# Performance work log

Hardware: AMD Instinct MI355X
Metric: run time of the kernel (lower is better)

## Reference

```python
import jax, jax.numpy as jnp
import numpy as np

B, L, C, K = 4, 32768, 64, 7
NORM_FACTOR = 1.0
EPS = 1e-5


def setup_inputs() -> dict:
    key = jax.random.key(0)
    ks = jax.random.split(key, 7)
    return {
        "x": jax.random.normal(ks[0], (B, L, C), jnp.float32),
        "weights": jax.random.normal(ks[1], (C, C, K), jnp.float32) * 0.05,  # ~lecun scale
        "w_conv": jax.random.normal(ks[2], (C, C), jnp.float32) * 0.125,
        "scale1": jax.random.uniform(ks[3], (C,), jnp.float32, 0.5, 1.5),
        "bias1": jax.random.normal(ks[4], (C,), jnp.float32) * 0.1,
        "scale2": jax.random.uniform(ks[5], (C,), jnp.float32, 0.5, 1.5),
        "bias2": jax.random.normal(ks[6], (C,), jnp.float32) * 0.1,
    }


def _batchnorm(x, scale, bias):
    # train-mode BatchNorm: stats over (batch, length), feature axis last
    mean = jnp.mean(x, axis=(0, 1), keepdims=True)
    var = jnp.var(x, axis=(0, 1), keepdims=True)
    return (x - mean) * jax.lax.rsqrt(var + EPS) * scale + bias


def reference(x, weights, w_conv, scale1, bias1, scale2, bias2):
    b, l, c = x.shape
    k = weights.shape[-1]
    x_ = x
    # unfold: windows of 2K at stride 2 -> (B, C*2K, T) -> (B, C, T, 2K)
    p = jax.lax.conv_general_dilated_patches(
        jnp.transpose(x, (0, 2, 1)), filter_shape=(2 * k,),
        window_strides=(2,), padding=((0, 0),))
    t = p.shape[-1]
    xp = jnp.transpose(jnp.reshape(p, (b, c, 2 * k, t)), (0, 1, 3, 2))
    # dynamic gate weights: (B, 2T, C) x (Cout, Cin, K) -> (B, Cout, 2T, K)
    w = jnp.einsum('blc,dck->bdlk', x_[:, -(2 * t):, :], weights)
    even_seq = w[:, :, ::2, :]   # (B, C, T, K)
    odd_seq = w[:, :, 1::2, :]   # (B, C, T, K)
    w = jnp.reshape(jnp.stack([even_seq, odd_seq], axis=-1), (b, c, t, 2 * k))
    w = jnp.tanh(w / NORM_FACTOR)
    y = jnp.sum(xp * w, axis=3)            # (B, C, T)
    y = jnp.transpose(y, (0, 2, 1))        # (B, T, C)
    y = x_[:, ::2, :][:, -t:, :] + y       # skip and inner_skip
    y = _batchnorm(y, scale1, bias1)
    y_ = y
    z = y @ w_conv                          # 1x1 conv, no bias
    z = _batchnorm(z, scale2, bias2)
    z = jax.nn.gelu(z)                      # approximate=True, matches flax default
    return y_ + z
```

## Files before the change

kernel.cpp:

```cpp
#include <hip/hip_runtime.h>
#include <hip/hip_bf16.h>

#define B_ 4
#define L_ 32768
#define C_ 64
#define K_ 7
#define T_ 16378
#define M_ (B_*T_)
#define TJ 16
#define IT 4
#define NJB 256
#define NBLKA (B_*NJB)
#define NBZ 512
#define NBE 1024

#define OF_WB   0
#define OF_WB2  14336
#define OF_Y    16384
#define OF_PS1  (OF_Y + M_*32)
#define OF_PQ1  (OF_PS1 + 64*NBLKA)
#define OF_PS2  (OF_PQ1 + 64*NBLKA)
#define OF_PQ2  (OF_PS2 + 64*NBZ)
#define OF_C1   (OF_PQ2 + 64*NBZ)
#define OF_C2   (OF_C1 + 128)

typedef __attribute__((ext_vector_type(8))) short short8;
typedef __attribute__((ext_vector_type(4))) float f32x4;

__device__ __forceinline__ unsigned cvt_pk_bf16(float a, float b) {
    unsigned r;
    asm("v_cvt_pk_bf16_f32 %0, %1, %2" : "=v"(r) : "v"(a), "v"(b));
    return r;
}

__device__ __forceinline__ float fast_tanh(float x) {
    float e = __builtin_amdgcn_exp2f(x * 2.885390082f);
    return __builtin_fmaf(-2.f, __builtin_amdgcn_rcpf(1.f + e), 1.f);
}

__device__ __forceinline__ float gelu_tanh(float v) {
    float u = 0.7978845608028654f * (v + 0.044715f * v * v * v);
    return 0.5f * v * (1.f + fast_tanh(u));
}

__device__ __forceinline__ float bfu(ushort h) {
    union { unsigned u; float f; } v; v.u = ((unsigned)h) << 16; return v.f;
}
__device__ __forceinline__ float bflo(unsigned p) {
    union { unsigned u; float f; } v; v.u = p << 16; return v.f;
}

__global__ void kPb(const float* __restrict__ w, ushort* __restrict__ Wb) {
    int i = blockIdx.x * 256 + threadIdx.x;
    if (i < 28672) {
        int j = i & 7;
        int l = (i >> 3) & 63;
        int q = i >> 9;
        int nt = q % 28, kt = q / 28;
        int k = kt * 32 + 8 * (l >> 4) + j;
        int n = nt * 16 + (l & 15);
        int d = n / 7, kk = n - 7 * d;
        Wb[i] = (ushort)(cvt_pk_bf16(w[(d * 64 + k) * 7 + kk], 0.f) & 0xffffu);
    }
}

__global__ __launch_bounds__(256, 4) void kA(const float* __restrict__ x,
                                             const ushort* __restrict__ Wb,
                                             ushort* __restrict__ y,
                                             float* __restrict__ ps,
                                             float* __restrict__ pq) {
    __shared__ ushort xp[22 * 128];
    __shared__ ushort gsT[448 * 36];
    __shared__ float  red[2][4][64];

    const int tid = threadIdx.x;
    const int w = tid >> 6, l = tid & 63;
    const int b = blockIdx.y;
    const float* xb = x + (long)b * L_ * 64;

    short8 wreg[7][2];
    #pragma unroll
    for (int i = 0; i < 7; ++i) {
        wreg[i][0] = *(const short8*)&Wb[((w + 4 * i) * 64 + l) * 8];
        wreg[i][1] = *(const short8*)&Wb[((28 + w + 4 * i) * 64 + l) * 8];
    }

    float S = 0.f, Q = 0.f;

    for (int it = 0; it < IT; ++it) {
        const int jt = blockIdx.x * IT + it;
        const int j0 = jt * TJ;
        const int xrow0 = 2 * j0;
        if (it) __syncthreads();

        #pragma unroll
        for (int st = 0; st < 3; ++st) {
            int p = tid + st * 256;
            if (p < 704) {
                int rp = p >> 5, c0 = (p & 31) * 2;
                int r0 = min(xrow0 + 2 * rp, L_ - 1);
                int r1 = min(xrow0 + 2 * rp + 1, L_ - 1);
                float2 va = *(const float2*)(xb + (long)r0 * 64 + c0);
                float2 vb = *(const float2*)(xb + (long)r1 * 64 + c0);
                uint2 wv;
                wv.x = cvt_pk_bf16(va.x, vb.x);
                wv.y = cvt_pk_bf16(va.y, vb.y);
                *(uint2*)((char*)xp + rp * 256 + c0 * 4) = wv;
            }
        }

        short8 afr[2][2];
        #pragma unroll
        for (int mt = 0; mt < 2; ++mt)
            #pragma unroll
            for (int kt = 0; kt < 2; ++kt) {
                int row = min(xrow0 + 12 + mt * 16 + (l & 15), L_ - 1);
                const float* pr = xb + (long)row * 64 + kt * 32 + (l >> 4) * 8;
                float4 v0 = *(const float4*)pr;
                float4 v1 = *(const float4*)(pr + 4);
                uint4 u;
                u.x = cvt_pk_bf16(v0.x, v0.y);
                u.y = cvt_pk_bf16(v0.z, v0.w);
                u.z = cvt_pk_bf16(v1.x, v1.y);
                u.w = cvt_pk_bf16(v1.z, v1.w);
                afr[mt][kt] = *(short8*)&u;
            }

        {
            const int col = l & 15;
            const int r0 = 4 * (l >> 4);
            #pragma unroll
            for (int i = 0; i < 7; ++i) {
                const int nt = w + 4 * i;
                f32x4 acc0 = {0.f, 0.f, 0.f, 0.f};
                f32x4 acc1 = {0.f, 0.f, 0.f, 0.f};
                acc0 = __builtin_amdgcn_mfma_f32_16x16x32_bf16(afr[0][0], wreg[i][0], acc0, 0, 0, 0);
                acc0 = __builtin_amdgcn_mfma_f32_16x16x32_bf16(afr[0][1], wreg[i][1], acc0, 0, 0, 0);
                acc1 = __builtin_amdgcn_mfma_f32_16x16x32_bf16(afr[1][0], wreg[i][0], acc1, 0, 0, 0);
                acc1 = __builtin_amdgcn_mfma_f32_16x16x32_bf16(afr[1][1], wreg[i][1], acc1, 0, 0, 0);
                const int n = nt * 16 + col;
                char* base = (char*)gsT + n * 72;
                uint2 lo, hi;
                lo.x = cvt_pk_bf16(fast_tanh(acc0[0]), fast_tanh(acc0[1]));
                lo.y = cvt_pk_bf16(fast_tanh(acc0[2]), fast_tanh(acc0[3]));
                hi.x = cvt_pk_bf16(fast_tanh(acc1[0]), fast_tanh(acc1[1]));
                hi.y = cvt_pk_bf16(fast_tanh(acc1[2]), fast_tanh(acc1[3]));
                *(uint2*)(base + r0 * 2)      = lo;
                *(uint2*)(base + 32 + r0 * 2) = hi;
            }
        }
        __syncthreads();

        #pragma unroll
        for (int jp = 0; jp < 2; ++jp) {
            const int jj0 = 2 * w + 8 * jp;
            unsigned xv[8];
            #pragma unroll
            for (int k2 = 0; k2 < 8; ++k2)
                xv[k2] = *(const unsigned*)((const char*)xp + (jj0 + k2) * 256 + l * 4);
            float acc0 = bflo(xv[6]);
            float acc1 = bflo(xv[7]);
            const char* gbp = (const char*)gsT + l * 504 + jj0 * 4;
            #pragma unroll
            for (int kk = 0; kk < K_; ++kk) {
                uint2 gp = *(const uint2*)(gbp + kk * 72);
                asm("v_dot2_f32_bf16 %0, %1, %2, %0" : "+v"(acc0) : "v"(xv[kk]),     "v"(gp.x));
                asm("v_dot2_f32_bf16 %0, %1, %2, %0" : "+v"(acc1) : "v"(xv[kk + 1]), "v"(gp.y));
            }
            float o0 = __shfl_xor(acc0, 1);
            float o1 = __shfl_xor(acc1, 1);
            const int j = j0 + jj0;
            if (j < T_) {
                if ((l & 1) == 0) {
                    *(unsigned*)((char*)y + (long)(b * T_ + j) * 128 + l * 2)     = cvt_pk_bf16(acc0, o0);
                    *(unsigned*)((char*)y + (long)(b * T_ + j + 1) * 128 + l * 2) = cvt_pk_bf16(acc1, o1);
                }
                S += acc0 + acc1;
                Q += acc0 * acc0 + acc1 * acc1;
            }
        }
    }

    red[0][w][l] = S;
    red[1][w][l] = Q;
    __syncthreads();
    if (tid < 64) {
        float S4 = red[0][0][tid] + red[0][1][tid] + red[0][2][tid] + red[0][3][tid];
        float Q4 = red[1][0][tid] + red[1][1][tid] + red[1][2][tid] + red[1][3][tid];
        int blk = b * NJB + blockIdx.x;
        ps[tid * NBLKA + blk] = S4;
        pq[tid * NBLKA + blk] = Q4;
    }
}

__global__ void kB(const float* __restrict__ ps, const float* __restrict__ pq,
                   float* __restrict__ A, float* __restrict__ BB,
                   const float* __restrict__ scale, const float* __restrict__ bias,
                   int nblk, float invN) {
    const int c = blockIdx.x;
    const float* bs = ps + (long)c * nblk;
    const float* bq = pq + (long)c * nblk;
    float S = 0.f, Q = 0.f;
    for (int i = threadIdx.x; i < nblk; i += 256) {
        S += bs[i];
        Q += bq[i];
    }
    for (int o = 32; o > 0; o >>= 1) {
        S += __shfl_down(S, o);
        Q += __shfl_down(Q, o);
    }
    __shared__ float rs[4], rq[4];
    if ((threadIdx.x & 63) == 0) { rs[threadIdx.x >> 6] = S; rq[threadIdx.x >> 6] = Q; }
    __syncthreads();
    if (threadIdx.x == 0) {
        S = rs[0] + rs[1] + rs[2] + rs[3];
        Q = rq[0] + rq[1] + rq[2] + rq[3];
        float m = S * invN;
        float var = Q * invN - m * m;
        float rstd = rsqrtf(var + 1e-5f);
        float a = rstd * scale[c];
        A[c] = a;
        BB[c] = bias[c] - m * a;
    }
}

__global__ void kW(const float* __restrict__ wconv, const float* __restrict__ A1,
                   ushort* __restrict__ Wb2) {
    int i = blockIdx.x * 256 + threadIdx.x;
    if (i < 4096) {
        int j = i & 7, lane = (i >> 3) & 63, q2 = i >> 9;
        int kt = q2 >> 2, nt = q2 & 3;
        int c = kt * 32 + 8 * (lane >> 4) + j;
        int e = nt * 16 + (lane & 15);
        Wb2[i] = (ushort)(cvt_pk_bf16(A1[c] * wconv[c * 64 + e], 0.f) & 0xffffu);
    }
}

__global__ __launch_bounds__(256) void kZ(const ushort* __restrict__ y,
                                          const ushort* __restrict__ Wb2,
                                          float* __restrict__ ps2,
                                          float* __restrict__ pq2) {
    __shared__ float red[2][4][64];
    const int tid = threadIdx.x, w = tid >> 6, l = tid & 63;
    short8 bfr[4][2];
    #pragma unroll
    for (int nt = 0; nt < 4; ++nt)
        #pragma unroll
        for (int kt = 0; kt < 2; ++kt)
            bfr[nt][kt] = *(const short8*)&Wb2[((kt * 4 + nt) * 64 + l) * 8];

    float ss[4] = {0.f, 0.f, 0.f, 0.f}, qq[4] = {0.f, 0.f, 0.f, 0.f};
    #pragma unroll
    for (int g2 = 0; g2 < 2; ++g2) {
        long rowg = (long)blockIdx.x * 128 + g2 * 64 + w * 16 + (l & 15);
        short8 a0 = {0, 0, 0, 0, 0, 0, 0, 0};
        short8 a1 = {0, 0, 0, 0, 0, 0, 0, 0};
        if (rowg < M_) {
            const char* yr = (const char*)y + rowg * 128 + (l >> 4) * 16;
            a0 = *(const short8*)yr;
            a1 = *(const short8*)(yr + 64);
        }
        #pragma unroll
        for (int nt = 0; nt < 4; ++nt) {
            f32x4 acc = {0.f, 0.f, 0.f, 0.f};
            acc = __builtin_amdgcn_mfma_f32_16x16x32_bf16(a0, bfr[nt][0], acc, 0, 0, 0);
            acc = __builtin_amdgcn_mfma_f32_16x16x32_bf16(a1, bfr[nt][1], acc, 0, 0, 0);
            #pragma unroll
            for (int i = 0; i < 4; ++i) { ss[nt] += acc[i]; qq[nt] += acc[i] * acc[i]; }
        }
    }
    #pragma unroll
    for (int nt = 0; nt < 4; ++nt) {
        float s2 = ss[nt] + __shfl_xor(ss[nt], 16); s2 += __shfl_xor(s2, 32);
        float q2 = qq[nt] + __shfl_xor(qq[nt], 16); q2 += __shfl_xor(q2, 32);
        if (l < 16) { red[0][w][nt * 16 + l] = s2; red[1][w][nt * 16 + l] = q2; }
    }
    __syncthreads();
    if (tid < 64) {
        float S = red[0][0][tid] + red[0][1][tid] + red[0][2][tid] + red[0][3][tid];
        float Q = red[1][0][tid] + red[1][1][tid] + red[1][2][tid] + red[1][3][tid];
        ps2[tid * NBZ + blockIdx.x] = S;
        pq2[tid * NBZ + blockIdx.x] = Q;
    }
}

__global__ __launch_bounds__(256) void kE(const ushort* __restrict__ y,
                                          const ushort* __restrict__ Wb2,
                                          const float* __restrict__ A1,
                                          const float* __restrict__ B1,
                                          const float* __restrict__ A2,
                                          const float* __restrict__ B2,
                                          float* __restrict__ out) {
    __shared__ float zs[64][68];
    __shared__ float cf[4][64];
    const int tid = threadIdx.x, w = tid >> 6, l = tid & 63;

    if (tid < 64)       cf[0][tid] = A1[tid];
    else if (tid < 128) cf[1][tid - 64] = B1[tid - 64];
    else if (tid < 192) cf[2][tid - 128] = A2[tid - 128];
    else                cf[3][tid - 192] = B2[tid - 192];

    short8 bfr[4][2];
    #pragma unroll
    for (int nt = 0; nt < 4; ++nt)
        #pragma unroll
        for (int kt = 0; kt < 2; ++kt)
            bfr[nt][kt] = *(const short8*)&Wb2[((kt * 4 + nt) * 64 + l) * 8];

    const long row0 = (long)blockIdx.x * 64;
    long rowg = row0 + w * 16 + (l & 15);
    short8 a0 = {0, 0, 0, 0, 0, 0, 0, 0};
    short8 a1 = {0, 0, 0, 0, 0, 0, 0, 0};
    if (rowg < M_) {
        const char* yr = (const char*)y + rowg * 128 + (l >> 4) * 16;
        a0 = *(const short8*)yr;
        a1 = *(const short8*)(yr + 64);
    }
    #pragma unroll
    for (int nt = 0; nt < 4; ++nt) {
        f32x4 acc = {0.f, 0.f, 0.f, 0.f};
        acc = __builtin_amdgcn_mfma_f32_16x16x32_bf16(a0, bfr[nt][0], acc, 0, 0, 0);
        acc = __builtin_amdgcn_mfma_f32_16x16x32_bf16(a1, bfr[nt][1], acc, 0, 0, 0);
        const int e = nt * 16 + (l & 15);
        #pragma unroll
        for (int i = 0; i < 4; ++i)
            zs[w * 16 + 4 * (l >> 4) + i][e] = acc[i];
    }
    __syncthreads();

    #pragma unroll
    for (int i = 0; i < 4; ++i) {
        int rloc = i * 16 + (tid >> 4);
        long gr = row0 + rloc;
        int ch0 = (tid & 15) * 4;
        if (gr < M_) {
            uint2 yp = *(const uint2*)((const char*)y + gr * 128 + ch0 * 2);
            float4 z4 = *(const float4*)&zs[rloc][ch0];
            float yv0 = bflo(yp.x), yv1 = bfu((ushort)(yp.x >> 16));
            float yv2 = bflo(yp.y), yv3 = bfu((ushort)(yp.y >> 16));
            float4 o;
            o.x = fmaf(cf[0][ch0 + 0], yv0, cf[1][ch0 + 0]) + gelu_tanh(fmaf(cf[2][ch0 + 0], z4.x, cf[3][ch0 + 0]));
            o.y = fmaf(cf[0][ch0 + 1], yv1, cf[1][ch0 + 1]) + gelu_tanh(fmaf(cf[2][ch0 + 1], z4.y, cf[3][ch0 + 1]));
            o.z = fmaf(cf[0][ch0 + 2], yv2, cf[1][ch0 + 2]) + gelu_tanh(fmaf(cf[2][ch0 + 2], z4.z, cf[3][ch0 + 2]));
            o.w = fmaf(cf[0][ch0 + 3], yv3, cf[1][ch0 + 3]) + gelu_tanh(fmaf(cf[2][ch0 + 3], z4.w, cf[3][ch0 + 3]));
            *(float4*)&out[gr * 64 + ch0] = o;
        }
    }
}

extern "C" void kernel_launch(void* const* d_in, const int* in_sizes, int n_in,
                              void* d_out, int out_size, void* d_ws, size_t ws_size,
                              hipStream_t stream) {
    const float* x       = (const float*)d_in[0];
    const float* weights = (const float*)d_in[1];
    const float* w_conv  = (const float*)d_in[2];
    const float* scale1  = (const float*)d_in[3];
    const float* bias1   = (const float*)d_in[4];
    const float* scale2  = (const float*)d_in[5];
    const float* bias2   = (const float*)d_in[6];
    float* out = (float*)d_out;
    float* ws  = (float*)d_ws;

    ushort* Wb  = (ushort*)(ws + OF_WB);
    ushort* Wb2 = (ushort*)(ws + OF_WB2);
    ushort* yb  = (ushort*)(ws + OF_Y);
    float* ps1 = ws + OF_PS1;
    float* pq1 = ws + OF_PQ1;
    float* ps2 = ws + OF_PS2;
    float* pq2 = ws + OF_PQ2;
    float* A1  = ws + OF_C1;
    float* BB1 = ws + OF_C1 + 64;
    float* A2  = ws + OF_C2;
    float* BB2 = ws + OF_C2 + 64;

    const float invN = 1.f / (float)M_;

    kPb<<<112, 256, 0, stream>>>(weights, Wb);
    kA<<<dim3(NJB, B_), 256, 0, stream>>>(x, Wb, yb, ps1, pq1);
    kB<<<64, 256, 0, stream>>>(ps1, pq1, A1, BB1, scale1, bias1, NBLKA, invN);
    kW<<<16, 256, 0, stream>>>(w_conv, A1, Wb2);
    kZ<<<NBZ, 256, 0, stream>>>(yb, Wb2, ps2, pq2);
    kB<<<64, 256, 0, stream>>>(ps2, pq2, A2, BB2, scale2, bias2, NBZ, invN);
    kE<<<NBE, 256, 0, stream>>>(yb, Wb2, A1, BB1, A2, BB2, out);
}
```

Baseline: 59.21 us.

## Software-prefetch next tile's global loads into registers in kA

Kernel kA now issues the next iteration's global loads of x into registers before the MFMA and tanh work of the current tile, so memory latency can overlap compute. It also merges the shared-memory buffers so the reduction array reuses the xp/gsT space, shrinking LDS use per block. Other changes are small: address math moves to 32-bit and min clamps apply only on the tail tile. The cost is extra VGPR pressure from holding prefetched float2/float4 values, which could hurt occupancy under launch_bounds(256,4).

```diff
diff --git a/kernel.cpp b/kernel.cpp
--- a/kernel.cpp
+++ b/kernel.cpp
@@ -69,14 +69,15 @@
                                              ushort* __restrict__ y,
                                              float* __restrict__ ps,
                                              float* __restrict__ pq) {
-    __shared__ ushort xp[22 * 128];
-    __shared__ ushort gsT[448 * 36];
-    __shared__ float  red[2][4][64];
+    __shared__ char sm[22 * 128 * 2 + 448 * 36 * 2];
+    ushort* xp  = (ushort*)sm;
+    ushort* gsT = (ushort*)(sm + 22 * 128 * 2);
+    float*  red = (float*)sm;
 
     const int tid = threadIdx.x;
     const int w = tid >> 6, l = tid & 63;
     const int b = blockIdx.y;
-    const float* xb = x + (long)b * L_ * 64;
+    const float* xb = x + b * (L_ * 64);
 
     short8 wreg[7][2];
     #pragma unroll
@@ -85,26 +86,51 @@
         wreg[i][1] = *(const short8*)&Wb[((28 + w + 4 * i) * 64 + l) * 8];
     }
 
+    float2 sva[3], svb[3];
+    float4 af0[2][2], af1[2][2];
+
+    auto issue_loads = [&](int jt) {
+        const int xrow0 = jt * (2 * TJ);
+        const bool tail = (jt == NJB * IT - 1);
+        #pragma unroll
+        for (int st = 0; st < 3; ++st) {
+            int p = tid + st * 256;
+            if (st < 2 || tid < 192) {
+                int rp = p >> 5, c0 = (p & 31) * 2;
+                int r0 = xrow0 + 2 * rp, r1 = r0 + 1;
+                if (tail) { r0 = min(r0, L_ - 1); r1 = min(r1, L_ - 1); }
+                sva[st] = *(const float2*)(xb + r0 * 64 + c0);
+                svb[st] = *(const float2*)(xb + r1 * 64 + c0);
+            }
+        }
+        #pragma unroll
+        for (int mt = 0; mt < 2; ++mt)
+            #pragma unroll
+            for (int kt = 0; kt < 2; ++kt) {
+                int row = xrow0 + 12 + mt * 16 + (l & 15);
+                if (tail) row = min(row, L_ - 1);
+                const float* pr = xb + row * 64 + kt * 32 + (l >> 4) * 8;
+                af0[mt][kt] = *(const float4*)pr;
+                af1[mt][kt] = *(const float4*)(pr + 4);
+            }
+    };
+
+    issue_loads(blockIdx.x * IT);
+
     float S = 0.f, Q = 0.f;
 
     for (int it = 0; it < IT; ++it) {
         const int jt = blockIdx.x * IT + it;
         const int j0 = jt * TJ;
-        const int xrow0 = 2 * j0;
-        if (it) __syncthreads();
 
         #pragma unroll
         for (int st = 0; st < 3; ++st) {
             int p = tid + st * 256;
-            if (p < 704) {
+            if (st < 2 || tid < 192) {
                 int rp = p >> 5, c0 = (p & 31) * 2;
-                int r0 = min(xrow0 + 2 * rp, L_ - 1);
-                int r1 = min(xrow0 + 2 * rp + 1, L_ - 1);
-                float2 va = *(const float2*)(xb + (long)r0 * 64 + c0);
-                float2 vb = *(const float2*)(xb + (long)r1 * 64 + c0);
                 uint2 wv;
-                wv.x = cvt_pk_bf16(va.x, vb.x);
-                wv.y = cvt_pk_bf16(va.y, vb.y);
+                wv.x = cvt_pk_bf16(sva[st].x, svb[st].x);
+                wv.y = cvt_pk_bf16(sva[st].y, svb[st].y);
                 *(uint2*)((char*)xp + rp * 256 + c0 * 4) = wv;
             }
         }
@@ -114,17 +140,15 @@
         for (int mt = 0; mt < 2; ++mt)
             #pragma unroll
             for (int kt = 0; kt < 2; ++kt) {
-                int row = min(xrow0 + 12 + mt * 16 + (l & 15), L_ - 1);
-                const float* pr = xb + (long)row * 64 + kt * 32 + (l >> 4) * 8;
-                float4 v0 = *(const float4*)pr;
-                float4 v1 = *(const float4*)(pr + 4);
                 uint4 u;
-                u.x = cvt_pk_bf16(v0.x, v0.y);
-                u.y = cvt_pk_bf16(v0.z, v0.w);
-                u.z = cvt_pk_bf16(v1.x, v1.y);
-                u.w = cvt_pk_bf16(v1.z, v1.w);
+                u.x = cvt_pk_bf16(af0[mt][kt].x, af0[mt][kt].y);
+                u.y = cvt_pk_bf16(af0[mt][kt].z, af0[mt][kt].w);
+                u.z = cvt_pk_bf16(af1[mt][kt].x, af1[mt][kt].y);
+                u.w = cvt_pk_bf16(af1[mt][kt].z, af1[mt][kt].w);
                 afr[mt][kt] = *(short8*)&u;
             }
+
+        if (it + 1 < IT) issue_loads(jt + 1);
 
         {
             const int col = l & 15;
@@ -172,21 +196,24 @@
             const int j = j0 + jj0;
             if (j < T_) {
                 if ((l & 1) == 0) {
-                    *(unsigned*)((char*)y + (long)(b * T_ + j) * 128 + l * 2)     = cvt_pk_bf16(acc0, o0);
-                    *(unsigned*)((char*)y + (long)(b * T_ + j + 1) * 128 + l * 2) = cvt_pk_bf16(acc1, o1);
+                    *(unsigned*)((char*)y + (b * T_ + j) * 128 + l * 2)       = cvt_pk_bf16(acc0, o0);
+                    *(unsigned*)((char*)y + (b * T_ + j + 1) * 128 + l * 2)   = cvt_pk_bf16(acc1, o1);
                 }
                 S += acc0 + acc1;
                 Q += acc0 * acc0 + acc1 * acc1;
             }
         }
-    }
-
-    red[0][w][l] = S;
-    red[1][w][l] = Q;
+        __syncthreads();
+    }
+
+    red[(0 * 4 + w) * 64 + l] = S;
+    red[(1 * 4 + w) * 64 + l] = Q;
     __syncthreads();
     if (tid < 64) {
-        float S4 = red[0][0][tid] + red[0][1][tid] + red[0][2][tid] + red[0][3][tid];
-        float Q4 = red[1][0][tid] + red[1][1][tid] + red[1][2][tid] + red[1][3][tid];
+        float S4 = red[0 * 256 + 0 * 64 + tid] + red[0 * 256 + 1 * 64 + tid]
+                 + red[0 * 256 + 2 * 64 + tid] + red[0 * 256 + 3 * 64 + tid];
+        float Q4 = red[1 * 256 + 0 * 64 + tid] + red[1 * 256 + 1 * 64 + tid]
+                 + red[1 * 256 + 2 * 64 + tid] + red[1 * 256 + 3 * 64 + tid];
         int blk = b * NJB + blockIdx.x;
         ps[tid * NBLKA + blk] = S4;
         pq[tid * NBLKA + blk] = Q4;
```

Result: slower. 69.47 us (+17.3%).

## Give each wave its own output channels to remove block barriers in kA

Applied to the files above, without the earlier changes.

Reassigns kernel A so that each wave owns 16 output channels. The wave computes the 7 gate tiles for those channels (using a new Wb indexing), stages its own slice of x and its gate values in private LDS regions, and reads them back without any __syncthreads. The final stats reduction now uses cross-lane shuffles instead of an LDS reduction plus a barrier, and row clamping is applied only on the last tile. The cost is that x loading becomes narrower scalar loads per wave, and the LDS layout is padded differently, which may change bank conflicts.

```diff
diff --git a/kernel.cpp b/kernel.cpp
--- a/kernel.cpp
+++ b/kernel.cpp
@@ -69,43 +69,42 @@
                                              ushort* __restrict__ y,
                                              float* __restrict__ ps,
                                              float* __restrict__ pq) {
-    __shared__ ushort xp[22 * 128];
-    __shared__ ushort gsT[448 * 36];
-    __shared__ float  red[2][4][64];
+    __shared__ char sm[4 * 7616 + 4 * 1496];
 
     const int tid = threadIdx.x;
     const int w = tid >> 6, l = tid & 63;
+    char* gw  = sm + w * 7616;
+    char* xpw = sm + 4 * 7616 + w * 1496;
     const int b = blockIdx.y;
-    const float* xb = x + (long)b * L_ * 64;
+    const float* xb = x + b * (L_ * 64);
 
     short8 wreg[7][2];
     #pragma unroll
     for (int i = 0; i < 7; ++i) {
-        wreg[i][0] = *(const short8*)&Wb[((w + 4 * i) * 64 + l) * 8];
-        wreg[i][1] = *(const short8*)&Wb[((28 + w + 4 * i) * 64 + l) * 8];
-    }
-
+        wreg[i][0] = *(const short8*)&Wb[((7 * w + i) * 64 + l) * 8];
+        wreg[i][1] = *(const short8*)&Wb[((28 + 7 * w + i) * 64 + l) * 8];
+    }
+
+    const int cl = l & 15, r0 = 4 * (l >> 4);
+    const int g = l >> 4, dp = l & 15;
     float S = 0.f, Q = 0.f;
 
     for (int it = 0; it < IT; ++it) {
         const int jt = blockIdx.x * IT + it;
         const int j0 = jt * TJ;
         const int xrow0 = 2 * j0;
-        if (it) __syncthreads();
-
-        #pragma unroll
-        for (int st = 0; st < 3; ++st) {
-            int p = tid + st * 256;
-            if (p < 704) {
-                int rp = p >> 5, c0 = (p & 31) * 2;
-                int r0 = min(xrow0 + 2 * rp, L_ - 1);
-                int r1 = min(xrow0 + 2 * rp + 1, L_ - 1);
-                float2 va = *(const float2*)(xb + (long)r0 * 64 + c0);
-                float2 vb = *(const float2*)(xb + (long)r1 * 64 + c0);
-                uint2 wv;
-                wv.x = cvt_pk_bf16(va.x, vb.x);
-                wv.y = cvt_pk_bf16(va.y, vb.y);
-                *(uint2*)((char*)xp + rp * 256 + c0 * 4) = wv;
+        const bool tail = (jt == NJB * IT - 1);
+
+        #pragma unroll
+        for (int q = 0; q < 6; ++q) {
+            int idx = q * 64 + l;
+            int rp = idx >> 4, c = idx & 15;
+            if (rp < 22) {
+                int ra = xrow0 + 2 * rp, rb = ra + 1;
+                if (tail) { ra = min(ra, L_ - 1); rb = min(rb, L_ - 1); }
+                float va = xb[ra * 64 + 16 * w + c];
+                float vb = xb[rb * 64 + 16 * w + c];
+                *(unsigned*)(xpw + rp * 68 + c * 4) = cvt_pk_bf16(va, vb);
             }
         }
 
@@ -114,8 +113,9 @@
         for (int mt = 0; mt < 2; ++mt)
             #pragma unroll
             for (int kt = 0; kt < 2; ++kt) {
-                int row = min(xrow0 + 12 + mt * 16 + (l & 15), L_ - 1);
-                const float* pr = xb + (long)row * 64 + kt * 32 + (l >> 4) * 8;
+                int row = xrow0 + 12 + mt * 16 + cl;
+                if (tail) row = min(row, L_ - 1);
+                const float* pr = xb + row * 64 + kt * 32 + (l >> 4) * 8;
                 float4 v0 = *(const float4*)pr;
                 float4 v1 = *(const float4*)(pr + 4);
                 uint4 u;
@@ -126,54 +126,45 @@
                 afr[mt][kt] = *(short8*)&u;
             }
 
-        {
-            const int col = l & 15;
-            const int r0 = 4 * (l >> 4);
-            #pragma unroll
-            for (int i = 0; i < 7; ++i) {
-                const int nt = w + 4 * i;
-                f32x4 acc0 = {0.f, 0.f, 0.f, 0.f};
-                f32x4 acc1 = {0.f, 0.f, 0.f, 0.f};
-                acc0 = __builtin_amdgcn_mfma_f32_16x16x32_bf16(afr[0][0], wreg[i][0], acc0, 0, 0, 0);
-                acc0 = __builtin_amdgcn_mfma_f32_16x16x32_bf16(afr[0][1], wreg[i][1], acc0, 0, 0, 0);
-                acc1 = __builtin_amdgcn_mfma_f32_16x16x32_bf16(afr[1][0], wreg[i][0], acc1, 0, 0, 0);
-                acc1 = __builtin_amdgcn_mfma_f32_16x16x32_bf16(afr[1][1], wreg[i][1], acc1, 0, 0, 0);
-                const int n = nt * 16 + col;
-                char* base = (char*)gsT + n * 72;
-                uint2 lo, hi;
-                lo.x = cvt_pk_bf16(fast_tanh(acc0[0]), fast_tanh(acc0[1]));
-                lo.y = cvt_pk_bf16(fast_tanh(acc0[2]), fast_tanh(acc0[3]));
-                hi.x = cvt_pk_bf16(fast_tanh(acc1[0]), fast_tanh(acc1[1]));
-                hi.y = cvt_pk_bf16(fast_tanh(acc1[2]), fast_tanh(acc1[3]));
-                *(uint2*)(base + r0 * 2)      = lo;
-                *(uint2*)(base + 32 + r0 * 2) = hi;
-            }
-        }
-        __syncthreads();
-
-        #pragma unroll
-        for (int jp = 0; jp < 2; ++jp) {
-            const int jj0 = 2 * w + 8 * jp;
+        #pragma unroll
+        for (int i = 0; i < 7; ++i) {
+            f32x4 acc0 = {0.f, 0.f, 0.f, 0.f};
+            f32x4 acc1 = {0.f, 0.f, 0.f, 0.f};
+            acc0 = __builtin_amdgcn_mfma_f32_16x16x32_bf16(afr[0][0], wreg[i][0], acc0, 0, 0, 0);
+            acc0 = __builtin_amdgcn_mfma_f32_16x16x32_bf16(afr[0][1], wreg[i][1], acc0, 0, 0, 0);
+            acc1 = __builtin_amdgcn_mfma_f32_16x16x32_bf16(afr[1][0], wreg[i][0], acc1, 0, 0, 0);
+            acc1 = __builtin_amdgcn_mfma_f32_16x16x32_bf16(afr[1][1], wreg[i][1], acc1, 0, 0, 0);
+            char* base = gw + (i * 16 + cl) * 68 + r0 * 2;
+            *(unsigned*)(base)      = cvt_pk_bf16(fast_tanh(acc0[0]), fast_tanh(acc0[1]));
+            *(unsigned*)(base + 4)  = cvt_pk_bf16(fast_tanh(acc0[2]), fast_tanh(acc0[3]));
+            *(unsigned*)(base + 32) = cvt_pk_bf16(fast_tanh(acc1[0]), fast_tanh(acc1[1]));
+            *(unsigned*)(base + 36) = cvt_pk_bf16(fast_tanh(acc1[2]), fast_tanh(acc1[3]));
+        }
+
+        #pragma unroll
+        for (int p = 0; p < 2; ++p) {
+            const int jj0 = 2 * g + 8 * p;
             unsigned xv[8];
             #pragma unroll
             for (int k2 = 0; k2 < 8; ++k2)
-                xv[k2] = *(const unsigned*)((const char*)xp + (jj0 + k2) * 256 + l * 4);
+                xv[k2] = *(const unsigned*)(xpw + (jj0 + k2) * 68 + dp * 4);
             float acc0 = bflo(xv[6]);
             float acc1 = bflo(xv[7]);
-            const char* gbp = (const char*)gsT + l * 504 + jj0 * 4;
+            const char* gb = gw + dp * 476 + jj0 * 4;
             #pragma unroll
             for (int kk = 0; kk < K_; ++kk) {
-                uint2 gp = *(const uint2*)(gbp + kk * 72);
-                asm("v_dot2_f32_bf16 %0, %1, %2, %0" : "+v"(acc0) : "v"(xv[kk]),     "v"(gp.x));
-                asm("v_dot2_f32_bf16 %0, %1, %2, %0" : "+v"(acc1) : "v"(xv[kk + 1]), "v"(gp.y));
+                unsigned g0 = *(const unsigned*)(gb + kk * 68);
+                unsigned g1 = *(const unsigned*)(gb + kk * 68 + 4);
+                asm("v_dot2_f32_bf16 %0, %1, %2, %0" : "+v"(acc0) : "v"(xv[kk]),     "v"(g0));
+                asm("v_dot2_f32_bf16 %0, %1, %2, %0" : "+v"(acc1) : "v"(xv[kk + 1]), "v"(g1));
             }
             float o0 = __shfl_xor(acc0, 1);
             float o1 = __shfl_xor(acc1, 1);
             const int j = j0 + jj0;
             if (j < T_) {
-                if ((l & 1) == 0) {
-                    *(unsigned*)((char*)y + (long)(b * T_ + j) * 128 + l * 2)     = cvt_pk_bf16(acc0, o0);
-                    *(unsigned*)((char*)y + (long)(b * T_ + j + 1) * 128 + l * 2) = cvt_pk_bf16(acc1, o1);
+                if ((dp & 1) == 0) {
+                    *(unsigned*)((char*)y + (b * T_ + j) * 128 + (16 * w + dp) * 2)     = cvt_pk_bf16(acc0, o0);
+                    *(unsigned*)((char*)y + (b * T_ + j + 1) * 128 + (16 * w + dp) * 2) = cvt_pk_bf16(acc1, o1);
                 }
                 S += acc0 + acc1;
                 Q += acc0 * acc0 + acc1 * acc1;
@@ -181,15 +172,13 @@
         }
     }
 
-    red[0][w][l] = S;
-    red[1][w][l] = Q;
-    __syncthreads();
-    if (tid < 64) {
-        float S4 = red[0][0][tid] + red[0][1][tid] + red[0][2][tid] + red[0][3][tid];
-        float Q4 = red[1][0][tid] + red[1][1][tid] + red[1][2][tid] + red[1][3][tid];
+    S += __shfl_xor(S, 16); S += __shfl_xor(S, 32);
+    Q += __shfl_xor(Q, 16); Q += __shfl_xor(Q, 32);
+    if (l < 16) {
+        int d = 16 * w + l;
         int blk = b * NJB + blockIdx.x;
-        ps[tid * NBLKA + blk] = S4;
-        pq[tid * NBLKA + blk] = Q4;
+        ps[d * NBLKA + blk] = S;
+        pq[d * NBLKA + blk] = Q;
     }
 }
 
```

Result: faster. 56.79 us (-4.1%).
